# Kernel tuning notes

Measured on AMD Instinct MI355X. Metric: run time of the kernel, lower is better.

The kernel has to match this reference:

```python
import math
import jax, jax.numpy as jnp
import numpy as np

B, L, D = 8, 512, 32
SEQ_LEN = 512.0
N_PATCHES, N_REF = 16, 32
LAT, HM = 128, 4
FH, NL, FF = 8, 3, 128
PRED = 96

def _time_embed(t, d):
    # interleaved sin/cos embedding, matching PositionalEmbedding's div_term
    div = jnp.exp(jnp.arange(0, d, 2, dtype=jnp.float32) * (-math.log(10000.0) / d))
    ang = t[..., None] * div
    out = jnp.zeros(t.shape + (d,), dtype=jnp.float32)
    return out.at[..., 0::2].set(jnp.sin(ang)).at[..., 1::2].set(jnp.cos(ang))

def _layernorm(x, g, b):
    mu = jnp.mean(x, axis=-1, keepdims=True)
    var = jnp.var(x, axis=-1, keepdims=True)
    return (x - mu) / jnp.sqrt(var + 1e-5) * g + b

def _mha(z, Wq, Wk, Wv, Wo, bq, bk, bv, bo):
    N, S, dm = z.shape
    hd = dm // FH
    q = (z @ Wq + bq).reshape(N, S, FH, hd)
    k = (z @ Wk + bk).reshape(N, S, FH, hd)
    v = (z @ Wv + bv).reshape(N, S, FH, hd)
    s = jnp.einsum('nqhe,nkhe->nhqk', q, k) / math.sqrt(hd)
    a = jax.nn.softmax(s, axis=-1)
    o = jnp.einsum('nhqk,nkhe->nqhe', a, v).reshape(N, S, dm)
    return o @ Wo + bo

def _forward(x, x_mark, x_mask, Wq, Wk, W_out, b_out, f_Wq, f_Wk, f_Wv, f_Wo, f_bq, f_bk, f_bv, f_bo, f_ln1_g, f_ln1_b, f_W1, f_b1, f_W2, f_b2, f_ln2_g, f_ln2_b, ln_f_g, ln_f_b, W_lin, b_lin):
    t = x_mark[:, :, 0]                                   # [B, L] irregular timestamps in [0, SEQ_LEN]
    edges = jnp.linspace(0.0, SEQ_LEN, N_PATCHES + 1)
    refs = jnp.linspace(0.0, SEQ_LEN, N_REF * N_PATCHES).reshape(N_PATCHES, N_REF)
    obs_valid = jnp.sum(x_mask, axis=-1) > 0              # [B, L]
    dk = LAT // HM
    Kmat = (_time_embed(t, LAT) @ Wk).reshape(B, L, HM, dk)
    v = x * x_mask                                        # mask values like `v = v * m` in original
    reprs = []
    for i in range(N_PATCHES):  # fixed small structural loop
        # _split_patch equivalent: per-channel masked attention is permutation
        # invariant, so the sort/scatter compaction reduces to masking.
        in_patch = (t >= edges[i]) & (t <= edges[i + 1]) & obs_valid   # [B, L]
        Qi = (_time_embed(refs[i], LAT) @ Wq).reshape(N_REF, HM, dk)
        scores = jnp.einsum('rhe,blhe->bhrl', Qi, Kmat) / math.sqrt(dk)
        cmask = x_mask * in_patch[..., None].astype(x.dtype)           # [B, L, D]
        neg = jnp.where(cmask[:, None, None, :, :] > 0, 0.0, -1e9)     # [B,1,1,L,D]
        p = jax.nn.softmax(scores[..., None] + neg, axis=3)            # [B,H,R,L,D]
        attn = jnp.einsum('bhrld,bld->brhd', p, v)                     # [B,R,H,D]
        reprs.append(attn.reshape(B, N_REF, HM * D) @ W_out + b_out)   # [B,R,D]
    rp = jnp.stack(reprs, axis=1)                          # [B, NP, R, D]
    z = rp.transpose(0, 3, 1, 2).reshape(B * D, N_PATCHES, N_REF)
    z = z + _time_embed(jnp.arange(N_PATCHES, dtype=jnp.float32), N_REF)[None]
    for l in range(NL):
        a = _mha(z, f_Wq[l], f_Wk[l], f_Wv[l], f_Wo[l], f_bq[l], f_bk[l], f_bv[l], f_bo[l])
        z = _layernorm(z + a, f_ln1_g[l], f_ln1_b[l])
        y = jax.nn.gelu(z @ f_W1[l] + f_b1[l]) @ f_W2[l] + f_b2[l]
        z = _layernorm(z + y, f_ln2_g[l], f_ln2_b[l])
    z = _layernorm(z, ln_f_g, ln_f_b)
    emb = z.reshape(B, D, N_PATCHES, N_REF).transpose(0, 1, 3, 2)      # [B, D, R, NP]
    out = emb.reshape(B, D, N_REF * N_PATCHES) @ W_lin + b_lin         # [B, D, PRED]
    return out.transpose(0, 2, 1)                          # [B, PRED, D]

def setup_inputs():
    key = jax.random.key(0)
    ks = jax.random.split(key, 30)
    def w(i, shape, fan_in):
        return jax.random.normal(ks[i], shape, jnp.float32) / math.sqrt(fan_in)
    return {
        'x': jax.random.normal(ks[0], (B, L, D), jnp.float32),
        'x_mark': jnp.sort(jax.random.uniform(ks[1], (B, L, 1), jnp.float32) * SEQ_LEN, axis=1),
        'x_mask': (jax.random.uniform(ks[2], (B, L, D), jnp.float32) < 0.8).astype(jnp.float32),
        'Wq': w(3, (LAT, LAT), LAT),
        'Wk': w(4, (LAT, LAT), LAT),
        'W_out': w(5, (HM * D, D), HM * D),
        'b_out': jnp.zeros((D,), jnp.float32),
        'f_Wq': w(6, (NL, N_REF, N_REF), N_REF),
        'f_Wk': w(7, (NL, N_REF, N_REF), N_REF),
        'f_Wv': w(8, (NL, N_REF, N_REF), N_REF),
        'f_Wo': w(9, (NL, N_REF, N_REF), N_REF),
        'f_bq': jnp.zeros((NL, N_REF), jnp.float32),
        'f_bk': jnp.zeros((NL, N_REF), jnp.float32),
        'f_bv': jnp.zeros((NL, N_REF), jnp.float32),
        'f_bo': jnp.zeros((NL, N_REF), jnp.float32),
        'f_ln1_g': jnp.ones((NL, N_REF), jnp.float32),
        'f_ln1_b': jnp.zeros((NL, N_REF), jnp.float32),
        'f_W1': w(10, (NL, N_REF, FF), N_REF),
        'f_b1': jnp.zeros((NL, FF), jnp.float32),
        'f_W2': w(11, (NL, FF, N_REF), FF),
        'f_b2': jnp.zeros((NL, N_REF), jnp.float32),
        'f_ln2_g': jnp.ones((NL, N_REF), jnp.float32),
        'f_ln2_b': jnp.zeros((NL, N_REF), jnp.float32),
        'ln_f_g': jnp.ones((N_REF,), jnp.float32),
        'ln_f_b': jnp.zeros((N_REF,), jnp.float32),
        'W_lin': w(12, (N_REF * N_PATCHES, PRED), N_REF * N_PATCHES),
        'b_lin': jnp.zeros((PRED,), jnp.float32),
    }

def reference(x, x_mark, x_mask, Wq, Wk, W_out, b_out, f_Wq, f_Wk, f_Wv, f_Wo, f_bq, f_bk, f_bv, f_bo, f_ln1_g, f_ln1_b, f_W1, f_b1, f_W2, f_b2, f_ln2_g, f_ln2_b, ln_f_g, ln_f_b, W_lin, b_lin):
    return _forward(x, x_mark, x_mask, Wq, Wk, W_out, b_out, f_Wq, f_Wk, f_Wv, f_Wo, f_bq, f_bk, f_bv, f_bo, f_ln1_g, f_ln1_b, f_W1, f_b1, f_W2, f_b2, f_ln2_g, f_ln2_b, ln_f_g, ln_f_b, W_lin, b_lin)
```

## Files before the change

kernel.cpp:

```cpp
#include <hip/hip_runtime.h>
#include <math.h>


#define ISQ32 0.17677669529663687f
#define C128  (-0.07195578415606394f)
#define C32   (-0.28782313662425575f)

__global__ void k_embed_mm(const float* __restrict__ x_mark,
                           const float* __restrict__ Wk,
                           const float* __restrict__ Wq,
                           const float* __restrict__ x_mask,
                           float* __restrict__ Kmat,
                           float* __restrict__ Qall,
                           unsigned* __restrict__ obsBits) {
    __shared__ float sTe[4][128];
    if (blockIdx.x >= 1152) {
        const int gt = (blockIdx.x - 1152) * 256 + threadIdx.x;
        const int w = gt >> 6, lane = gt & 63;
        const int bl = w * 2 + (lane >> 5);
        const int d = lane & 31;
        const unsigned long long mm = __ballot(x_mask[bl * 32 + d] > 0.0f);
        if (lane == 0)  obsBits[w * 2]     = (unsigned)(mm & 0xffffffffull);
        if (lane == 32) obsBits[w * 2 + 1] = (unsigned)(mm >> 32);
        return;
    }
    const int wave = threadIdx.x >> 6;
    const int lane = threadIdx.x & 63;
    const int row = blockIdx.x * 4 + wave;
    float t;
    const float* W;
    float* outp;
    if (row < 4096) {
        t = x_mark[row];
        W = Wk;
        outp = Kmat + row * 128;
    } else {
        const int qr = row - 4096;
        t = (float)qr * (512.0f / 511.0f);
        W = Wq;
        outp = Qall + qr * 128;
    }
    const float dv = expf((float)(2 * lane) * C128);
    const float ang = t * dv;
    sTe[wave][2 * lane]     = sinf(ang);
    sTe[wave][2 * lane + 1] = cosf(ang);
    __syncthreads();
    float a0 = 0.f, a1 = 0.f;
    #pragma unroll 8
    for (int k = 0; k < 128; ++k) {
        const float te = sTe[wave][k];
        a0 = fmaf(te, W[k * 128 + lane], a0);
        a1 = fmaf(te, W[k * 128 + lane + 64], a1);
    }
    outp[lane] = a0;
    outp[lane + 64] = a1;
}

__launch_bounds__(256)
__global__ void k_patch_attn(const float* __restrict__ x,
                             const float* __restrict__ x_mark,
                             const unsigned* __restrict__ obsBits,
                             const float* __restrict__ Kmat,
                             const float* __restrict__ Qall,
                             float* __restrict__ attn) {
    __shared__ float sQ[32][36];
    __shared__ float sK[96][36];
    __shared__ float sX[96][36];
    __shared__ float sS[32][100];
    __shared__ unsigned sBits[96];
    __shared__ int sLo, sHi;
    __shared__ unsigned sAV;
    const int tid = threadIdx.x;
    const int h = blockIdx.x & 3;
    const int b = (blockIdx.x >> 2) & 7;
    const int i = blockIdx.x >> 5;
    const float e0 = 32.0f * (float)i, e1 = 32.0f * (float)(i + 1);
    if (tid == 0) { sLo = 512; sHi = -1; sAV = 0u; }
    __syncthreads();
    #pragma unroll
    for (int k = 0; k < 4; ++k) {
        const int idx = tid + 256 * k;
        sQ[idx >> 5][idx & 31] = Qall[(i * 32 + (idx >> 5)) * 128 + h * 32 + (idx & 31)];
    }
    {
        int mylo = 512, myhi = -1;
        unsigned mybits = 0u;
        #pragma unroll
        for (int k = 0; k < 2; ++k) {
            const int l = tid + 256 * k;
            const float t = x_mark[b * 512 + l];
            if (t >= e0 && t <= e1) {
                mylo = min(mylo, l);
                myhi = max(myhi, l);
                mybits |= obsBits[b * 512 + l];
            }
        }
        #pragma unroll
        for (int off = 32; off > 0; off >>= 1) {
            mylo = min(mylo, __shfl_xor(mylo, off));
            myhi = max(myhi, __shfl_xor(myhi, off));
            mybits |= __shfl_xor(mybits, off);
        }
        if ((tid & 63) == 0) {
            atomicMin(&sLo, mylo);
            atomicMax(&sHi, myhi);
            atomicOr(&sAV, mybits);
        }
    }
    __syncthreads();
    const int lo = sLo, hi = sHi;
    const int NA = hi - lo + 1;
    const unsigned av = sAV;
    const int r = tid >> 3, dg = tid & 7;

    if (NA >= 1 && NA <= 96 && av == 0xffffffffu) {
        if (tid < NA) sBits[tid] = obsBits[b * 512 + lo + tid];
        for (int idx = tid; idx < NA * 32; idx += 256) {
            const int ll = idx >> 5, c = idx & 31;
            sK[ll][c] = Kmat[(b * 512 + lo + ll) * 128 + h * 32 + c];
            sX[ll][c] = x[(b * 512 + lo + ll) * 32 + c];
        }
        __syncthreads();
        float m = -1e30f;
        for (int ll = dg; ll < NA; ll += 8) {
            float p0 = 0.f, p1 = 0.f, p2 = 0.f, p3 = 0.f;
            #pragma unroll
            for (int e = 0; e < 32; e += 4) {
                p0 = fmaf(sQ[r][e],     sK[ll][e],     p0);
                p1 = fmaf(sQ[r][e + 1], sK[ll][e + 1], p1);
                p2 = fmaf(sQ[r][e + 2], sK[ll][e + 2], p2);
                p3 = fmaf(sQ[r][e + 3], sK[ll][e + 3], p3);
            }
            const float s = (p0 + p1 + p2 + p3) * ISQ32;
            sS[r][ll] = s;
            m = fmaxf(m, s);
        }
        #pragma unroll
        for (int off = 4; off > 0; off >>= 1) m = fmaxf(m, __shfl_xor(m, off));
        for (int ll = dg; ll < NA; ll += 8) sS[r][ll] = __expf(sS[r][ll] - m);
        __syncthreads();
        float num0 = 0.f, num1 = 0.f, num2 = 0.f, num3 = 0.f;
        float den0 = 0.f, den1 = 0.f, den2 = 0.f, den3 = 0.f;
        for (int ll = 0; ll < NA; ++ll) {
            const float e = sS[r][ll];
            const unsigned bits = sBits[ll];
            if ((bits >> dg) & 1u)        { den0 += e; num0 = fmaf(e, sX[ll][dg],      num0); }
            if ((bits >> (dg + 8)) & 1u)  { den1 += e; num1 = fmaf(e, sX[ll][dg + 8],  num1); }
            if ((bits >> (dg + 16)) & 1u) { den2 += e; num2 = fmaf(e, sX[ll][dg + 16], num2); }
            if ((bits >> (dg + 24)) & 1u) { den3 += e; num3 = fmaf(e, sX[ll][dg + 24], num3); }
        }
        float* ap = attn + ((i * 8 + b) * 32 + r) * 128 + h * 32;
        ap[dg]      = num0 / den0;
        ap[dg + 8]  = num1 / den1;
        ap[dg + 16] = num2 / den2;
        ap[dg + 24] = num3 / den3;
    } else {
        float m = -1e30f;
        float num[4] = {0.f, 0.f, 0.f, 0.f}, den[4] = {0.f, 0.f, 0.f, 0.f};
        for (int l = 0; l < 512; ++l) {
            const float t = x_mark[b * 512 + l];
            const unsigned bits = obsBits[b * 512 + l];
            const bool inr = (t >= e0 && t <= e1);
            const unsigned effD = (inr ? bits : 0u) | ~av;
            if (effD == 0u) continue;
            const unsigned effN = effD & bits;
            const float* Kp = Kmat + (b * 512 + l) * 128 + h * 32;
            float a = 0.f;
            #pragma unroll
            for (int e2 = 0; e2 < 32; ++e2) a = fmaf(sQ[r][e2], Kp[e2], a);
            const float s = a * ISQ32;
            float eNew;
            if (s > m) {
                const float scale = __expf(m - s);
                #pragma unroll
                for (int j = 0; j < 4; ++j) { den[j] *= scale; num[j] *= scale; }
                m = s;
                eNew = 1.0f;
            } else {
                eNew = __expf(s - m);
            }
            const float* xp = x + (b * 512 + l) * 32;
            #pragma unroll
            for (int j = 0; j < 4; ++j) {
                const int d = dg + 8 * j;
                if ((effD >> d) & 1u) den[j] += eNew;
                if ((effN >> d) & 1u) num[j] = fmaf(eNew, xp[d], num[j]);
            }
        }
        float* ap = attn + ((i * 8 + b) * 32 + r) * 128 + h * 32;
        #pragma unroll
        for (int j = 0; j < 4; ++j) ap[dg + 8 * j] = num[j] / den[j];
    }
}

__global__ void k_reprs(const float* __restrict__ attn,
                        const float* __restrict__ W_out,
                        const float* __restrict__ b_out,
                        float* __restrict__ z) {
    __shared__ float sA[32][129];
    const int tid = threadIdx.x;
    const int b = blockIdx.x & 7;
    const int i = blockIdx.x >> 3;
    #pragma unroll
    for (int k = 0; k < 16; ++k) {
        const int idx = tid + 256 * k;
        sA[idx >> 7][idx & 127] = attn[(i * 8 + b) * 4096 + idx];
    }
    __syncthreads();
    const int r = tid & 31, dgrp = tid >> 5;
    float acc0 = 0.f, acc1 = 0.f, acc2 = 0.f, acc3 = 0.f;
    #pragma unroll 8
    for (int k = 0; k < 128; ++k) {
        const float a = sA[r][k];
        acc0 = fmaf(a, W_out[k * 32 + dgrp],      acc0);
        acc1 = fmaf(a, W_out[k * 32 + dgrp + 8],  acc1);
        acc2 = fmaf(a, W_out[k * 32 + dgrp + 16], acc2);
        acc3 = fmaf(a, W_out[k * 32 + dgrp + 24], acc3);
    }
    const float dv = expf((float)(2 * (r >> 1)) * C32);
    const float ang = (float)i * dv;
    const float pe = (r & 1) ? cosf(ang) : sinf(ang);
    const int base = i * 32 + r;
    z[(b * 32 + dgrp)      * 512 + base] = acc0 + b_out[dgrp]      + pe;
    z[(b * 32 + dgrp + 8)  * 512 + base] = acc1 + b_out[dgrp + 8]  + pe;
    z[(b * 32 + dgrp + 16) * 512 + base] = acc2 + b_out[dgrp + 16] + pe;
    z[(b * 32 + dgrp + 24) * 512 + base] = acc3 + b_out[dgrp + 24] + pe;
}

__launch_bounds__(256)
__global__ void k_former(const float* __restrict__ z,
                         const float* __restrict__ f_Wq, const float* __restrict__ f_Wk,
                         const float* __restrict__ f_Wv, const float* __restrict__ f_Wo,
                         const float* __restrict__ f_bq, const float* __restrict__ f_bk,
                         const float* __restrict__ f_bv, const float* __restrict__ f_bo,
                         const float* __restrict__ f_ln1_g, const float* __restrict__ f_ln1_b,
                         const float* __restrict__ f_W1, const float* __restrict__ f_b1,
                         const float* __restrict__ f_W2, const float* __restrict__ f_b2,
                         const float* __restrict__ f_ln2_g, const float* __restrict__ f_ln2_b,
                         const float* __restrict__ ln_f_g, const float* __restrict__ ln_f_b,
                         const float* __restrict__ W_lin, const float* __restrict__ b_lin,
                         float* __restrict__ out) {
    __shared__ float sZ[16][33], sQ[16][33], sK[16][33], sV[16][33], sO[16][33], sT[16][33];
    __shared__ float sH[16][129];
    __shared__ float sWq[1024], sWk[1024], sWv[1024], sWo[1024];
    __shared__ float sW1[4096], sW2[4096];
    __shared__ float sBq[32], sBk[32], sBv[32], sBo[32], sB1[128], sB2[32];
    __shared__ float sL1g[32], sL1b[32], sL2g[32], sL2b[32];
    __shared__ float sZf[512];
    __shared__ float sPart[2][96];
    const int tid = threadIdx.x;
    const int n = blockIdx.x;
    #pragma unroll
    for (int k = 0; k < 2; ++k) {
        const int idx = tid + 256 * k;
        sZ[idx >> 5][idx & 31] = z[n * 512 + idx];
    }
    for (int layer = 0; layer < 3; ++layer) {
        ((float4*)sWq)[tid] = ((const float4*)(f_Wq + layer * 1024))[tid];
        ((float4*)sWk)[tid] = ((const float4*)(f_Wk + layer * 1024))[tid];
        ((float4*)sWv)[tid] = ((const float4*)(f_Wv + layer * 1024))[tid];
        ((float4*)sWo)[tid] = ((const float4*)(f_Wo + layer * 1024))[tid];
        #pragma unroll
        for (int k2 = 0; k2 < 4; ++k2) {
            ((float4*)sW1)[tid + 256 * k2] = ((const float4*)(f_W1 + layer * 4096))[tid + 256 * k2];
            ((float4*)sW2)[tid + 256 * k2] = ((const float4*)(f_W2 + layer * 4096))[tid + 256 * k2];
        }
        {
            const int j = tid & 31;
            switch (tid >> 5) {
                case 0: sBq[j]  = f_bq[layer * 32 + j];    break;
                case 1: sBk[j]  = f_bk[layer * 32 + j];    break;
                case 2: sBv[j]  = f_bv[layer * 32 + j];    break;
                case 3: sBo[j]  = f_bo[layer * 32 + j];    break;
                case 4: sB2[j]  = f_b2[layer * 32 + j];    break;
                case 5: sL1g[j] = f_ln1_g[layer * 32 + j]; break;
                case 6: sL1b[j] = f_ln1_b[layer * 32 + j]; break;
                case 7: sL2g[j] = f_ln2_g[layer * 32 + j]; break;
            }
            if (tid < 128) sB1[tid] = f_b1[layer * 128 + tid];
            else if (tid < 160) sL2b[tid - 128] = f_ln2_b[layer * 32 + (tid - 128)];
        }
        __syncthreads();
        #pragma unroll
        for (int it = 0; it < 6; ++it) {
            const int idx = tid + 256 * it;
            const int which = idx >> 9, rem = idx & 511, s = rem >> 5, j = rem & 31;
            const float* W  = (which == 0) ? sWq : ((which == 1) ? sWk : sWv);
            const float* bb = (which == 0) ? sBq : ((which == 1) ? sBk : sBv);
            float acc = bb[j];
            #pragma unroll
            for (int k = 0; k < 32; ++k) acc = fmaf(sZ[s][k], W[k * 32 + j], acc);
            if (which == 0) sQ[s][j] = acc;
            else if (which == 1) sK[s][j] = acc;
            else sV[s][j] = acc;
        }
        __syncthreads();
        if (tid < 128) {
            const int hh = tid >> 4, q = tid & 15;
            float sc[16];
            float mx = -1e30f;
            #pragma unroll
            for (int k = 0; k < 16; ++k) {
                float a = 0.f;
                #pragma unroll
                for (int e = 0; e < 4; ++e) a = fmaf(sQ[q][hh * 4 + e], sK[k][hh * 4 + e], a);
                sc[k] = a * 0.5f;
                mx = fmaxf(mx, sc[k]);
            }
            float sum = 0.f;
            #pragma unroll
            for (int k = 0; k < 16; ++k) { sc[k] = __expf(sc[k] - mx); sum += sc[k]; }
            const float inv = 1.0f / sum;
            #pragma unroll
            for (int e = 0; e < 4; ++e) {
                float a = 0.f;
                #pragma unroll
                for (int k = 0; k < 16; ++k) a = fmaf(sc[k], sV[k][hh * 4 + e], a);
                sO[q][hh * 4 + e] = a * inv;
            }
        }
        __syncthreads();
        #pragma unroll
        for (int it = 0; it < 2; ++it) {
            const int idx = tid + 256 * it, s = idx >> 5, j = idx & 31;
            float acc = sBo[j];
            #pragma unroll
            for (int k = 0; k < 32; ++k) acc = fmaf(sO[s][k], sWo[k * 32 + j], acc);
            sT[s][j] = sZ[s][j] + acc;
        }
        __syncthreads();
        {
            const int s = tid >> 4, g = tid & 15;
            const float v0 = sT[s][g], v1 = sT[s][g + 16];
            float sum = v0 + v1, sq = v0 * v0 + v1 * v1;
            #pragma unroll
            for (int off = 8; off > 0; off >>= 1) {
                sum += __shfl_xor(sum, off);
                sq  += __shfl_xor(sq, off);
            }
            const float mu = sum * (1.0f / 32.0f);
            const float rs = rsqrtf(sq * (1.0f / 32.0f) - mu * mu + 1e-5f);
            sZ[s][g]      = (v0 - mu) * rs * sL1g[g]      + sL1b[g];
            sZ[s][g + 16] = (v1 - mu) * rs * sL1g[g + 16] + sL1b[g + 16];
        }
        __syncthreads();
        #pragma unroll
        for (int it = 0; it < 8; ++it) {
            const int idx = tid + 256 * it, s = idx >> 7, f = idx & 127;
            float acc = sB1[f];
            #pragma unroll
            for (int k = 0; k < 32; ++k) acc = fmaf(sZ[s][k], sW1[k * 128 + f], acc);
            const float c = acc;
            const float a2 = 1.5957691216057308f * (c + 0.044715f * c * c * c);
            const float e = __expf(a2);
            const float th = 1.0f - 2.0f / (e + 1.0f);
            sH[s][f] = 0.5f * c * (1.0f + th);
        }
        __syncthreads();
        #pragma unroll
        for (int it = 0; it < 2; ++it) {
            const int idx = tid + 256 * it, s = idx >> 5, j = idx & 31;
            float acc = sB2[j];
            #pragma unroll 16
            for (int k = 0; k < 128; ++k) acc = fmaf(sH[s][k], sW2[k * 32 + j], acc);
            sT[s][j] = sZ[s][j] + acc;
        }
        __syncthreads();
        {
            const int s = tid >> 4, g = tid & 15;
            const float v0 = sT[s][g], v1 = sT[s][g + 16];
            float sum = v0 + v1, sq = v0 * v0 + v1 * v1;
            #pragma unroll
            for (int off = 8; off > 0; off >>= 1) {
                sum += __shfl_xor(sum, off);
                sq  += __shfl_xor(sq, off);
            }
            const float mu = sum * (1.0f / 32.0f);
            const float rs = rsqrtf(sq * (1.0f / 32.0f) - mu * mu + 1e-5f);
            sZ[s][g]      = (v0 - mu) * rs * sL2g[g]      + sL2b[g];
            sZ[s][g + 16] = (v1 - mu) * rs * sL2g[g + 16] + sL2b[g + 16];
        }
    }
    __syncthreads();
    {
        const int s = tid >> 4, g = tid & 15;
        const float v0 = sZ[s][g], v1 = sZ[s][g + 16];
        float sum = v0 + v1, sq = v0 * v0 + v1 * v1;
        #pragma unroll
        for (int off = 8; off > 0; off >>= 1) {
            sum += __shfl_xor(sum, off);
            sq  += __shfl_xor(sq, off);
        }
        const float mu = sum * (1.0f / 32.0f);
        const float rs = rsqrtf(sq * (1.0f / 32.0f) - mu * mu + 1e-5f);
        sZf[g * 16 + s]        = (v0 - mu) * rs * ln_f_g[g]      + ln_f_b[g];
        sZf[(g + 16) * 16 + s] = (v1 - mu) * rs * ln_f_g[g + 16] + ln_f_b[g + 16];
    }
    __syncthreads();
    if (tid < 192) {
        const int half = tid / 96, o = tid % 96;
        const int j0 = half * 256;
        float acc = 0.f;
        #pragma unroll 8
        for (int j = 0; j < 256; ++j)
            acc = fmaf(sZf[j0 + j], W_lin[(j0 + j) * 96 + o], acc);
        sPart[half][o] = acc;
    }
    __syncthreads();
    if (tid < 96)
        out[((n >> 5) * 96 + tid) * 32 + (n & 31)] = sPart[0][tid] + sPart[1][tid] + b_lin[tid];
}

extern "C" void kernel_launch(void* const* d_in, const int* in_sizes, int n_in,
                              void* d_out, int out_size, void* d_ws, size_t ws_size,
                              hipStream_t stream) {
    const float* x       = (const float*)d_in[0];
    const float* x_mark  = (const float*)d_in[1];
    const float* x_mask  = (const float*)d_in[2];
    const float* Wq      = (const float*)d_in[3];
    const float* Wk      = (const float*)d_in[4];
    const float* W_out   = (const float*)d_in[5];
    const float* b_out   = (const float*)d_in[6];
    const float* f_Wq    = (const float*)d_in[7];
    const float* f_Wk    = (const float*)d_in[8];
    const float* f_Wv    = (const float*)d_in[9];
    const float* f_Wo    = (const float*)d_in[10];
    const float* f_bq    = (const float*)d_in[11];
    const float* f_bk    = (const float*)d_in[12];
    const float* f_bv    = (const float*)d_in[13];
    const float* f_bo    = (const float*)d_in[14];
    const float* f_ln1_g = (const float*)d_in[15];
    const float* f_ln1_b = (const float*)d_in[16];
    const float* f_W1    = (const float*)d_in[17];
    const float* f_b1    = (const float*)d_in[18];
    const float* f_W2    = (const float*)d_in[19];
    const float* f_b2    = (const float*)d_in[20];
    const float* f_ln2_g = (const float*)d_in[21];
    const float* f_ln2_b = (const float*)d_in[22];
    const float* ln_f_g  = (const float*)d_in[23];
    const float* ln_f_b  = (const float*)d_in[24];
    const float* W_lin   = (const float*)d_in[25];
    const float* b_lin   = (const float*)d_in[26];

    float* ws = (float*)d_ws;
    float* Kmat      = ws;
    float* Qall      = ws + 524288;
    unsigned* obsB   = (unsigned*)(ws + 589824);
    float* attn      = ws + 593920;
    float* zbuf      = ws + 1118208;

    k_embed_mm<<<1664, 256, 0, stream>>>(x_mark, Wk, Wq, x_mask, Kmat, Qall, obsB);
    k_patch_attn<<<512, 256, 0, stream>>>(x, x_mark, obsB, Kmat, Qall, attn);
    k_reprs<<<128, 256, 0, stream>>>(attn, W_out, b_out, zbuf);
    k_former<<<256, 256, 0, stream>>>(zbuf,
        f_Wq, f_Wk, f_Wv, f_Wo, f_bq, f_bk, f_bv, f_bo,
        f_ln1_g, f_ln1_b, f_W1, f_b1, f_W2, f_b2, f_ln2_g, f_ln2_b,
        ln_f_g, ln_f_b, W_lin, b_lin, (float*)d_out);
}
```

Measured before the change: 77.45 us.

## Hold transformer weights in registers and fuse residual+layernorm into projections

The former kernel stops staging per-layer weight matrices and biases in shared memory. Each thread instead loads its weight column straight from global memory into registers and computes two sequence rows for Q/K/V, the output projection, FFN1 and FFN2. The residual add and layernorm are fused into the projection steps through 32-lane shuffles with the residual kept in registers, which removes the sT buffer and several barriers. The cost is heavy register use (w2c holds 128 floats), launch bounds of (256,1), and repeated global weight reads per block instead of a cooperative shared load.

```diff
diff --git a/kernel.cpp b/kernel.cpp
--- a/kernel.cpp
+++ b/kernel.cpp
@@ -227,7 +227,7 @@
     z[(b * 32 + dgrp + 24) * 512 + base] = acc3 + b_out[dgrp + 24] + pe;
 }
 
-__launch_bounds__(256)
+__launch_bounds__(256, 1)
 __global__ void k_former(const float* __restrict__ z,
                          const float* __restrict__ f_Wq, const float* __restrict__ f_Wk,
                          const float* __restrict__ f_Wv, const float* __restrict__ f_Wo,
@@ -240,59 +240,66 @@
                          const float* __restrict__ ln_f_g, const float* __restrict__ ln_f_b,
                          const float* __restrict__ W_lin, const float* __restrict__ b_lin,
                          float* __restrict__ out) {
-    __shared__ float sZ[16][33], sQ[16][33], sK[16][33], sV[16][33], sO[16][33], sT[16][33];
-    __shared__ float sH[16][129];
-    __shared__ float sWq[1024], sWk[1024], sWv[1024], sWo[1024];
-    __shared__ float sW1[4096], sW2[4096];
-    __shared__ float sBq[32], sBk[32], sBv[32], sBo[32], sB1[128], sB2[32];
-    __shared__ float sL1g[32], sL1b[32], sL2g[32], sL2b[32];
+    __shared__ float sZ[16][32];
+    __shared__ float sQ[16][33], sK[16][33], sV[16][33];
+    __shared__ float sO[16][32];
+    __shared__ float sH[16][128];
     __shared__ float sZf[512];
     __shared__ float sPart[2][96];
     const int tid = threadIdx.x;
     const int n = blockIdx.x;
+    const int j = tid & 31, s2 = tid >> 5;
+    const int sA = s2 * 2, sB = sA + 1;
+
     #pragma unroll
     for (int k = 0; k < 2; ++k) {
         const int idx = tid + 256 * k;
         sZ[idx >> 5][idx & 31] = z[n * 512 + idx];
     }
+    float zlocA = z[n * 512 + sA * 32 + j];
+    float zlocB = z[n * 512 + sB * 32 + j];
+    __syncthreads();
+
     for (int layer = 0; layer < 3; ++layer) {
-        ((float4*)sWq)[tid] = ((const float4*)(f_Wq + layer * 1024))[tid];
-        ((float4*)sWk)[tid] = ((const float4*)(f_Wk + layer * 1024))[tid];
-        ((float4*)sWv)[tid] = ((const float4*)(f_Wv + layer * 1024))[tid];
-        ((float4*)sWo)[tid] = ((const float4*)(f_Wo + layer * 1024))[tid];
-        #pragma unroll
-        for (int k2 = 0; k2 < 4; ++k2) {
-            ((float4*)sW1)[tid + 256 * k2] = ((const float4*)(f_W1 + layer * 4096))[tid + 256 * k2];
-            ((float4*)sW2)[tid + 256 * k2] = ((const float4*)(f_W2 + layer * 4096))[tid + 256 * k2];
-        }
+        const float* Wq = f_Wq + layer * 1024;
+        const float* Wk = f_Wk + layer * 1024;
+        const float* Wv = f_Wv + layer * 1024;
+        const float* Wo = f_Wo + layer * 1024;
+        const float* W1 = f_W1 + layer * 4096;
+        const float* W2 = f_W2 + layer * 4096;
+
         {
-            const int j = tid & 31;
-            switch (tid >> 5) {
-                case 0: sBq[j]  = f_bq[layer * 32 + j];    break;
-                case 1: sBk[j]  = f_bk[layer * 32 + j];    break;
-                case 2: sBv[j]  = f_bv[layer * 32 + j];    break;
-                case 3: sBo[j]  = f_bo[layer * 32 + j];    break;
-                case 4: sB2[j]  = f_b2[layer * 32 + j];    break;
-                case 5: sL1g[j] = f_ln1_g[layer * 32 + j]; break;
-                case 6: sL1b[j] = f_ln1_b[layer * 32 + j]; break;
-                case 7: sL2g[j] = f_ln2_g[layer * 32 + j]; break;
-            }
-            if (tid < 128) sB1[tid] = f_b1[layer * 128 + tid];
-            else if (tid < 160) sL2b[tid - 128] = f_ln2_b[layer * 32 + (tid - 128)];
-        }
-        __syncthreads();
-        #pragma unroll
-        for (int it = 0; it < 6; ++it) {
-            const int idx = tid + 256 * it;
-            const int which = idx >> 9, rem = idx & 511, s = rem >> 5, j = rem & 31;
-            const float* W  = (which == 0) ? sWq : ((which == 1) ? sWk : sWv);
-            const float* bb = (which == 0) ? sBq : ((which == 1) ? sBk : sBv);
-            float acc = bb[j];
-            #pragma unroll
-            for (int k = 0; k < 32; ++k) acc = fmaf(sZ[s][k], W[k * 32 + j], acc);
-            if (which == 0) sQ[s][j] = acc;
-            else if (which == 1) sK[s][j] = acc;
-            else sV[s][j] = acc;
+            float wq[32], wk[32], wv[32];
+            #pragma unroll
+            for (int k = 0; k < 32; ++k) {
+                wq[k] = Wq[k * 32 + j];
+                wk[k] = Wk[k * 32 + j];
+                wv[k] = Wv[k * 32 + j];
+            }
+            float qa = f_bq[layer * 32 + j], qb = qa;
+            float ka = f_bk[layer * 32 + j], kb = ka;
+            float va = f_bv[layer * 32 + j], vb = va;
+            const float4* zra = (const float4*)&sZ[sA][0];
+            const float4* zrb = (const float4*)&sZ[sB][0];
+            #pragma unroll
+            for (int k4 = 0; k4 < 8; ++k4) {
+                const float4 a = zra[k4], b4 = zrb[k4];
+                qa = fmaf(a.x, wq[4*k4], qa);   qa = fmaf(a.y, wq[4*k4+1], qa);
+                qa = fmaf(a.z, wq[4*k4+2], qa); qa = fmaf(a.w, wq[4*k4+3], qa);
+                qb = fmaf(b4.x, wq[4*k4], qb);   qb = fmaf(b4.y, wq[4*k4+1], qb);
+                qb = fmaf(b4.z, wq[4*k4+2], qb); qb = fmaf(b4.w, wq[4*k4+3], qb);
+                ka = fmaf(a.x, wk[4*k4], ka);   ka = fmaf(a.y, wk[4*k4+1], ka);
+                ka = fmaf(a.z, wk[4*k4+2], ka); ka = fmaf(a.w, wk[4*k4+3], ka);
+                kb = fmaf(b4.x, wk[4*k4], kb);   kb = fmaf(b4.y, wk[4*k4+1], kb);
+                kb = fmaf(b4.z, wk[4*k4+2], kb); kb = fmaf(b4.w, wk[4*k4+3], kb);
+                va = fmaf(a.x, wv[4*k4], va);   va = fmaf(a.y, wv[4*k4+1], va);
+                va = fmaf(a.z, wv[4*k4+2], va); va = fmaf(a.w, wv[4*k4+3], va);
+                vb = fmaf(b4.x, wv[4*k4], vb);   vb = fmaf(b4.y, wv[4*k4+1], vb);
+                vb = fmaf(b4.z, wv[4*k4+2], vb); vb = fmaf(b4.w, wv[4*k4+3], vb);
+            }
+            sQ[sA][j] = qa; sQ[sB][j] = qb;
+            sK[sA][j] = ka; sK[sB][j] = kb;
+            sV[sA][j] = va; sV[sB][j] = vb;
         }
         __syncthreads();
         if (tid < 128) {
@@ -320,81 +327,112 @@
             }
         }
         __syncthreads();
-        #pragma unroll
-        for (int it = 0; it < 2; ++it) {
-            const int idx = tid + 256 * it, s = idx >> 5, j = idx & 31;
-            float acc = sBo[j];
-            #pragma unroll
-            for (int k = 0; k < 32; ++k) acc = fmaf(sO[s][k], sWo[k * 32 + j], acc);
-            sT[s][j] = sZ[s][j] + acc;
-        }
-        __syncthreads();
         {
-            const int s = tid >> 4, g = tid & 15;
-            const float v0 = sT[s][g], v1 = sT[s][g + 16];
-            float sum = v0 + v1, sq = v0 * v0 + v1 * v1;
-            #pragma unroll
-            for (int off = 8; off > 0; off >>= 1) {
-                sum += __shfl_xor(sum, off);
-                sq  += __shfl_xor(sq, off);
-            }
-            const float mu = sum * (1.0f / 32.0f);
-            const float rs = rsqrtf(sq * (1.0f / 32.0f) - mu * mu + 1e-5f);
-            sZ[s][g]      = (v0 - mu) * rs * sL1g[g]      + sL1b[g];
-            sZ[s][g + 16] = (v1 - mu) * rs * sL1g[g + 16] + sL1b[g + 16];
-        }
-        __syncthreads();
-        #pragma unroll
-        for (int it = 0; it < 8; ++it) {
-            const int idx = tid + 256 * it, s = idx >> 7, f = idx & 127;
-            float acc = sB1[f];
-            #pragma unroll
-            for (int k = 0; k < 32; ++k) acc = fmaf(sZ[s][k], sW1[k * 128 + f], acc);
-            const float c = acc;
-            const float a2 = 1.5957691216057308f * (c + 0.044715f * c * c * c);
-            const float e = __expf(a2);
-            const float th = 1.0f - 2.0f / (e + 1.0f);
-            sH[s][f] = 0.5f * c * (1.0f + th);
-        }
-        __syncthreads();
-        #pragma unroll
-        for (int it = 0; it < 2; ++it) {
-            const int idx = tid + 256 * it, s = idx >> 5, j = idx & 31;
-            float acc = sB2[j];
-            #pragma unroll 16
-            for (int k = 0; k < 128; ++k) acc = fmaf(sH[s][k], sW2[k * 32 + j], acc);
-            sT[s][j] = sZ[s][j] + acc;
+            float wo[32];
+            #pragma unroll
+            for (int k = 0; k < 32; ++k) wo[k] = Wo[k * 32 + j];
+            float oa = f_bo[layer * 32 + j], ob = oa;
+            const float4* ora = (const float4*)&sO[sA][0];
+            const float4* orb = (const float4*)&sO[sB][0];
+            #pragma unroll
+            for (int k4 = 0; k4 < 8; ++k4) {
+                const float4 a = ora[k4], b4 = orb[k4];
+                oa = fmaf(a.x, wo[4*k4], oa);   oa = fmaf(a.y, wo[4*k4+1], oa);
+                oa = fmaf(a.z, wo[4*k4+2], oa); oa = fmaf(a.w, wo[4*k4+3], oa);
+                ob = fmaf(b4.x, wo[4*k4], ob);   ob = fmaf(b4.y, wo[4*k4+1], ob);
+                ob = fmaf(b4.z, wo[4*k4+2], ob); ob = fmaf(b4.w, wo[4*k4+3], ob);
+            }
+            const float tA = zlocA + oa, tB = zlocB + ob;
+            float sumA = tA, sqA = tA * tA, sumB = tB, sqB = tB * tB;
+            #pragma unroll
+            for (int off = 16; off > 0; off >>= 1) {
+                sumA += __shfl_xor(sumA, off); sqA += __shfl_xor(sqA, off);
+                sumB += __shfl_xor(sumB, off); sqB += __shfl_xor(sqB, off);
+            }
+            const float muA = sumA * (1.0f / 32.0f);
+            const float rsA = rsqrtf(sqA * (1.0f / 32.0f) - muA * muA + 1e-5f);
+            const float muB = sumB * (1.0f / 32.0f);
+            const float rsB = rsqrtf(sqB * (1.0f / 32.0f) - muB * muB + 1e-5f);
+            const float g1 = f_ln1_g[layer * 32 + j], be1 = f_ln1_b[layer * 32 + j];
+            zlocA = (tA - muA) * rsA * g1 + be1;
+            zlocB = (tB - muB) * rsB * g1 + be1;
+            sZ[sA][j] = zlocA;
+            sZ[sB][j] = zlocB;
         }
         __syncthreads();
         {
-            const int s = tid >> 4, g = tid & 15;
-            const float v0 = sT[s][g], v1 = sT[s][g + 16];
-            float sum = v0 + v1, sq = v0 * v0 + v1 * v1;
-            #pragma unroll
-            for (int off = 8; off > 0; off >>= 1) {
-                sum += __shfl_xor(sum, off);
-                sq  += __shfl_xor(sq, off);
-            }
-            const float mu = sum * (1.0f / 32.0f);
-            const float rs = rsqrtf(sq * (1.0f / 32.0f) - mu * mu + 1e-5f);
-            sZ[s][g]      = (v0 - mu) * rs * sL2g[g]      + sL2b[g];
-            sZ[s][g + 16] = (v1 - mu) * rs * sL2g[g + 16] + sL2b[g + 16];
-        }
-    }
-    __syncthreads();
+            const int f = tid & 127, sh = tid >> 7;
+            float w1c[32];
+            #pragma unroll
+            for (int k = 0; k < 32; ++k) w1c[k] = W1[k * 128 + f];
+            const float b1v = f_b1[layer * 128 + f];
+            #pragma unroll
+            for (int ss = 0; ss < 8; ++ss) {
+                const int s = sh * 8 + ss;
+                const float4* zr = (const float4*)&sZ[s][0];
+                float acc = b1v;
+                #pragma unroll
+                for (int k4 = 0; k4 < 8; ++k4) {
+                    const float4 a = zr[k4];
+                    acc = fmaf(a.x, w1c[4*k4], acc);   acc = fmaf(a.y, w1c[4*k4+1], acc);
+                    acc = fmaf(a.z, w1c[4*k4+2], acc); acc = fmaf(a.w, w1c[4*k4+3], acc);
+                }
+                const float c = acc;
+                const float a2 = 1.5957691216057308f * (c + 0.044715f * c * c * c);
+                const float e = __expf(a2);
+                const float th = 1.0f - 2.0f / (e + 1.0f);
+                sH[s][f] = 0.5f * c * (1.0f + th);
+            }
+        }
+        float w2c[128];
+        #pragma unroll
+        for (int k = 0; k < 128; ++k) w2c[k] = W2[k * 32 + j];
+        __syncthreads();
+        {
+            float fa = f_b2[layer * 32 + j], fb = fa;
+            const float4* hra = (const float4*)&sH[sA][0];
+            const float4* hrb = (const float4*)&sH[sB][0];
+            #pragma unroll
+            for (int k4 = 0; k4 < 32; ++k4) {
+                const float4 a = hra[k4], b4 = hrb[k4];
+                fa = fmaf(a.x, w2c[4*k4], fa);   fa = fmaf(a.y, w2c[4*k4+1], fa);
+                fa = fmaf(a.z, w2c[4*k4+2], fa); fa = fmaf(a.w, w2c[4*k4+3], fa);
+                fb = fmaf(b4.x, w2c[4*k4], fb);   fb = fmaf(b4.y, w2c[4*k4+1], fb);
+                fb = fmaf(b4.z, w2c[4*k4+2], fb); fb = fmaf(b4.w, w2c[4*k4+3], fb);
+            }
+            const float tA = zlocA + fa, tB = zlocB + fb;
+            float sumA = tA, sqA = tA * tA, sumB = tB, sqB = tB * tB;
+            #pragma unroll
+            for (int off = 16; off > 0; off >>= 1) {
+                sumA += __shfl_xor(sumA, off); sqA += __shfl_xor(sqA, off);
+                sumB += __shfl_xor(sumB, off); sqB += __shfl_xor(sqB, off);
+            }
+            const float muA = sumA * (1.0f / 32.0f);
+            const float rsA = rsqrtf(sqA * (1.0f / 32.0f) - muA * muA + 1e-5f);
+            const float muB = sumB * (1.0f / 32.0f);
+            const float rsB = rsqrtf(sqB * (1.0f / 32.0f) - muB * muB + 1e-5f);
+            const float g2 = f_ln2_g[layer * 32 + j], be2 = f_ln2_b[layer * 32 + j];
+            zlocA = (tA - muA) * rsA * g2 + be2;
+            zlocB = (tB - muB) * rsB * g2 + be2;
+            sZ[sA][j] = zlocA;
+            sZ[sB][j] = zlocB;
+        }
+        __syncthreads();
+    }
     {
-        const int s = tid >> 4, g = tid & 15;
-        const float v0 = sZ[s][g], v1 = sZ[s][g + 16];
-        float sum = v0 + v1, sq = v0 * v0 + v1 * v1;
-        #pragma unroll
-        for (int off = 8; off > 0; off >>= 1) {
-            sum += __shfl_xor(sum, off);
-            sq  += __shfl_xor(sq, off);
-        }
-        const float mu = sum * (1.0f / 32.0f);
-        const float rs = rsqrtf(sq * (1.0f / 32.0f) - mu * mu + 1e-5f);
-        sZf[g * 16 + s]        = (v0 - mu) * rs * ln_f_g[g]      + ln_f_b[g];
-        sZf[(g + 16) * 16 + s] = (v1 - mu) * rs * ln_f_g[g + 16] + ln_f_b[g + 16];
+        float sumA = zlocA, sqA = zlocA * zlocA, sumB = zlocB, sqB = zlocB * zlocB;
+        #pragma unroll
+        for (int off = 16; off > 0; off >>= 1) {
+            sumA += __shfl_xor(sumA, off); sqA += __shfl_xor(sqA, off);
+            sumB += __shfl_xor(sumB, off); sqB += __shfl_xor(sqB, off);
+        }
+        const float muA = sumA * (1.0f / 32.0f);
+        const float rsA = rsqrtf(sqA * (1.0f / 32.0f) - muA * muA + 1e-5f);
+        const float muB = sumB * (1.0f / 32.0f);
+        const float rsB = rsqrtf(sqB * (1.0f / 32.0f) - muB * muB + 1e-5f);
+        const float gf = ln_f_g[j], bf = ln_f_b[j];
+        sZf[j * 16 + sA] = (zlocA - muA) * rsA * gf + bf;
+        sZf[j * 16 + sB] = (zlocB - muB) * rsB * gf + bf;
     }
     __syncthreads();
     if (tid < 192) {
@@ -402,8 +440,8 @@
         const int j0 = half * 256;
         float acc = 0.f;
         #pragma unroll 8
-        for (int j = 0; j < 256; ++j)
-            acc = fmaf(sZf[j0 + j], W_lin[(j0 + j) * 96 + o], acc);
+        for (int jj = 0; jj < 256; ++jj)
+            acc = fmaf(sZf[j0 + jj], W_lin[(j0 + jj) * 96 + o], acc);
         sPart[half][o] = acc;
     }
     __syncthreads();
```

After: 70.36 us. -9.1%, faster.
